# Kernel optimization log

Measured on AMD Instinct MI355X. Metric: run time of the kernel, lower is better.

Reference implementation:

```python
import jax, jax.numpy as jnp
import numpy as np

EPS = 1e-5

def _bn_train(x, gamma, beta):
    # BatchNorm2d in training mode: batch stats over (N,H,W), biased variance
    mean = jnp.mean(x, axis=(0, 2, 3), keepdims=True)
    var = jnp.mean((x - mean) ** 2, axis=(0, 2, 3), keepdims=True)
    xn = (x - mean) / jnp.sqrt(var + EPS)
    return xn * gamma[None, :, None, None] + beta[None, :, None, None]

def _bin_act(x):
    # forward: sign(x); backward: grad of clamp(x,-1,1) (STE)
    c = jnp.clip(x, -1.0, 1.0)
    return jax.lax.stop_gradient(jnp.sign(x) - c) + c

def _bin_conv(x, w_flat, out_chn, in_chn, k=3, stride=1, padding=1):
    w = w_flat.reshape(out_chn, in_chn, k, k)
    scale = jax.lax.stop_gradient(jnp.mean(jnp.abs(w), axis=(1, 2, 3), keepdims=True))
    cw = jnp.clip(w, -1.0, 1.0)
    bw = jax.lax.stop_gradient(scale * jnp.sign(w) - cw) + cw
    return jax.lax.conv_general_dilated(
        x, bw, window_strides=(stride, stride),
        padding=[(padding, padding), (padding, padding)],
        dimension_numbers=('NCHW', 'OIHW', 'NCHW'))

def _prelu(x, a):
    return jnp.where(x >= 0, x, a * x)

def setup_inputs() -> dict:
    key = jax.random.key(0)
    ks = jax.random.split(key, 4)
    C = 128
    x = jax.random.normal(ks[0], (64, C, 56, 56), dtype=jnp.float32)
    # HardBinaryConv stores weights as (n,1); init small, mixed-sign
    w1 = (jax.random.uniform(ks[1], (C * C * 9, 1), dtype=jnp.float32) - 0.5) * 0.002
    w2 = (jax.random.uniform(ks[2], (C * C * 9, 1), dtype=jnp.float32) - 0.5) * 0.002
    ones = jnp.ones((C,), jnp.float32)
    zeros = jnp.zeros((C,), jnp.float32)
    a = jnp.float32(0.25)
    return {
        'x': x,
        'bn1_g': ones, 'bn1_b': zeros,
        'w1': w1, 'prelu1_a': a,
        'bn2_g': ones, 'bn2_b': zeros,
        'w2': w2, 'prelu2_a': a,
        'bn3_g': ones, 'bn3_b': zeros,
        'prelu3_a': a,
    }

def reference(x, bn1_g, bn1_b, w1, prelu1_a, bn2_g, bn2_b, w2, prelu2_a, bn3_g, bn3_b, prelu3_a):
    C = x.shape[1]
    out = _bn_train(x, bn1_g, bn1_b)
    out = _bin_act(out)
    out = _prelu(_bin_conv(out, w1, C, C), prelu1_a)
    out = _bn_train(out, bn2_g, bn2_b)
    out = _bin_act(out)
    out = _bin_conv(out, w2, C, C)
    out = _prelu(out, prelu2_a)
    out = _bn_train(out, bn3_g, bn3_b)
    out = out + x  # identity shortcut (stride=1, in_planes==planes)
    out = _prelu(out, prelu3_a)
    return out
```

## Files before the change

kernel.cpp:

```cpp
#include <hip/hip_runtime.h>
#include <hip/hip_bf16.h>

typedef __attribute__((ext_vector_type(8))) short short8;
typedef __attribute__((ext_vector_type(4))) int i32x4;

#define HW     3136
#define M_TOT  200704
#define NSTEP  18
#define NBLK   1568

__device__ __forceinline__ void gload_lds16(const void* g, void* l) {
    __builtin_amdgcn_global_load_lds(
        (const __attribute__((address_space(1))) void*)g,
        (__attribute__((address_space(3))) void*)l, 16, 0, 0);
}

__global__ __launch_bounds__(256) void wsign_kernel(const float* __restrict__ w1,
                                                    const float* __restrict__ w2,
                                                    char* __restrict__ ws1,
                                                    char* __restrict__ ws2) {
    int i = blockIdx.x * 256 + threadIdx.x;
    const float* w = w1;
    char* wsz = ws1;
    if (i >= 147456) { i -= 147456; w = w2; wsz = ws2; }
    int e = i & 15, l = (i >> 4) & 63, f = (i >> 10) & 7, s = i >> 13;
    int cout = f * 16 + (l & 15);
    int k = s * 64 + (l >> 4) * 16 + e;
    int tap = k >> 7, cin = k & 127;
    float v = w[(cout * 128 + cin) * 9 + tap];
    wsz[i] = v > 0.f ? (char)1 : (v < 0.f ? (char)-1 : (char)0);
}

__global__ __launch_bounds__(256) void wscale_kernel(const float* __restrict__ w1,
                                                     const float* __restrict__ w2,
                                                     float* __restrict__ scale1,
                                                     float* __restrict__ scale2) {
    int o = blockIdx.x;
    const float* w = w1;
    float* scale = scale1;
    if (o >= 128) { o -= 128; w = w2; scale = scale2; }
    int t = threadIdx.x;
    float s = 0.f;
    for (int i = t; i < 1152; i += 256) s += fabsf(w[o * 1152 + i]);
    __shared__ float r1[256];
    r1[t] = s; __syncthreads();
    for (int off = 128; off > 0; off >>= 1) {
        if (t < off) r1[t] += r1[t + off];
        __syncthreads();
    }
    if (t == 0) scale[o] = r1[0] * (1.f / 1152.f);
}

__global__ __launch_bounds__(256) void stats_nchw_kernel(const float* __restrict__ x,
                                                         float* __restrict__ psum,
                                                         float* __restrict__ psq) {
    int bid = blockIdx.x;
    int n = bid >> 7, c = bid & 127;
    const float* p = x + (n * 128 + c) * HW;
    int t = threadIdx.x;
    float s = 0.f, q = 0.f;
    for (int i = t; i < HW; i += 256) { float v = p[i]; s += v; q += v * v; }
    __shared__ float r1[256], r2[256];
    r1[t] = s; r2[t] = q; __syncthreads();
    for (int off = 128; off > 0; off >>= 1) {
        if (t < off) { r1[t] += r1[t + off]; r2[t] += r2[t + off]; }
        __syncthreads();
    }
    if (t == 0) { psum[c * 64 + n] = r1[0]; psq[c * 64 + n] = r2[0]; }
}

__global__ void finalize_kernel(const float* __restrict__ psum, const float* __restrict__ psq,
                                int P, float* __restrict__ mean, float* __restrict__ rstd) {
    int c = threadIdx.x;
    if (c >= 128) return;
    float s = 0.f, q = 0.f;
    for (int j = 0; j < P; ++j) { s += psum[c * P + j]; q += psq[c * P + j]; }
    const float invN = 1.f / 200704.f;
    float m = s * invN;
    float var = q * invN - m * m;
    mean[c] = m;
    rstd[c] = 1.f / sqrtf(var + 1e-5f);
}

__global__ __launch_bounds__(256) void finalizeB_kernel(const float* __restrict__ psumB,
                                                        const float* __restrict__ psqB,
                                                        float* __restrict__ mean,
                                                        float* __restrict__ rstd) {
    int c = blockIdx.x, t = threadIdx.x;
    float s = 0.f, q = 0.f;
    for (int j = t; j < NBLK; j += 256) { s += psumB[c * NBLK + j]; q += psqB[c * NBLK + j]; }
    __shared__ float r1[256], r2[256];
    r1[t] = s; r2[t] = q; __syncthreads();
    for (int off = 128; off > 0; off >>= 1) {
        if (t < off) { r1[t] += r1[t + off]; r2[t] += r2[t + off]; }
        __syncthreads();
    }
    if (t == 0) {
        const float invN = 1.f / 200704.f;
        float m = r1[0] * invN;
        float var = r2[0] * invN - m * m;
        mean[c] = m;
        rstd[c] = 1.f / sqrtf(var + 1e-5f);
    }
}

__global__ __launch_bounds__(256) void act1_kernel(const float* __restrict__ x,
        const float* __restrict__ mean, const float* __restrict__ rstd,
        const float* __restrict__ g, const float* __restrict__ b,
        char* __restrict__ apad) {
    __shared__ float row[128 * 57];
    int blk = blockIdx.x;
    int n = blk / 58, hp = blk - n * 58;
    char* o = apad + (n * 58 + hp) * 58 * 128;
    int t = threadIdx.x;
    if (hp == 0 || hp == 57) {
        for (int i4 = t; i4 < 58 * 32; i4 += 256)
            *(char4*)(o + i4 * 4) = make_char4(0, 0, 0, 0);
        return;
    }
    const float* src = x + n * (128 * HW) + (hp - 1) * 56;
    for (int i = t; i < 128 * 56; i += 256) {
        int c = i / 56, w = i - c * 56;
        row[c * 57 + w] = src[c * HW + w];
    }
    __syncthreads();
    for (int i4 = t; i4 < 58 * 32; i4 += 256) {
        int wp = i4 >> 5;
        int c0 = (i4 & 31) * 4;
        char q[4] = {0, 0, 0, 0};
        if (wp >= 1 && wp <= 56) {
#pragma unroll
            for (int k = 0; k < 4; ++k) {
                int c = c0 + k;
                float xn = (row[c * 57 + wp - 1] - mean[c]) * rstd[c] * g[c] + b[c];
                q[k] = xn > 0.f ? 1 : (xn < 0.f ? -1 : 0);
            }
        }
        *(char4*)(o + wp * 128 + c0) = make_char4(q[0], q[1], q[2], q[3]);
    }
}

__global__ __launch_bounds__(256) void act2_kernel(const short* __restrict__ p1,
        const float* __restrict__ scale1, const float* __restrict__ a1ptr,
        const float* __restrict__ mean, const float* __restrict__ rstd,
        const float* __restrict__ g, const float* __restrict__ b,
        char* __restrict__ apad) {
    __shared__ float row[128 * 57];
    int blk = blockIdx.x;
    int n = blk / 58, hp = blk - n * 58;
    char* o = apad + (n * 58 + hp) * 58 * 128;
    int t = threadIdx.x;
    if (hp == 0 || hp == 57) {
        for (int i4 = t; i4 < 58 * 32; i4 += 256)
            *(char4*)(o + i4 * 4) = make_char4(0, 0, 0, 0);
        return;
    }
    float a1 = a1ptr[0];
    const short* src = p1 + n * HW + (hp - 1) * 56;
    for (int i = t; i < 128 * 56; i += 256) {
        int c = i / 56, w = i - c * 56;
        float v = scale1[c] * (float)src[(size_t)c * M_TOT + w];
        row[c * 57 + w] = v >= 0.f ? v : a1 * v;
    }
    __syncthreads();
    for (int i4 = t; i4 < 58 * 32; i4 += 256) {
        int wp = i4 >> 5;
        int c0 = (i4 & 31) * 4;
        char q[4] = {0, 0, 0, 0};
        if (wp >= 1 && wp <= 56) {
#pragma unroll
            for (int k = 0; k < 4; ++k) {
                int c = c0 + k;
                float xn = (row[c * 57 + wp - 1] - mean[c]) * rstd[c] * g[c] + b[c];
                q[k] = xn > 0.f ? 1 : (xn < 0.f ? -1 : 0);
            }
        }
        *(char4*)(o + wp * 128 + c0) = make_char4(q[0], q[1], q[2], q[3]);
    }
}

__global__ __launch_bounds__(256, 3) void conv_kernel(
        const char* __restrict__ apad,
        const char* __restrict__ wswz,
        const float* __restrict__ scale,
        const float* __restrict__ aptr,
        short* __restrict__ obuf,
        float* __restrict__ psumB,
        float* __restrict__ psqB) {
    __shared__ __align__(1024) char lds[16384];
    char* ldsA = lds;
    char* ldsB = lds + 8192;

    const int tid = threadIdx.x;
    const int lane = tid & 63;
    const int wid = tid >> 6;
    const int l15 = lane & 15;
    const int lq = lane >> 4;
    const int wr = wid >> 1;
    const int wc = wid & 1;

    int bid = blockIdx.x;
    int mblk = (bid & 7) * 196 + (bid >> 3);
    const int m0 = mblk * 128;

    const char* bsrc[2];
#pragma unroll
    for (int j = 0; j < 2; ++j) {
        int m = m0 + (j * 4 + wid) * 16 + l15;
        int n = m / HW;
        int r = m - n * HW;
        int h = r / 56;
        int w = r - h * 56;
        bsrc[j] = apad + (((n * 58 + h) * 58 + w) * 128 + lq * 16);
    }

    i32x4 acc[4][4];
#pragma unroll
    for (int i = 0; i < 4; ++i)
#pragma unroll
        for (int j = 0; j < 4; ++j)
            acc[i][j] = (i32x4){0, 0, 0, 0};

    for (int s = 0; s < NSTEP; ++s) {
        int tap = s >> 1;
        int dh = tap / 3;
        int dw = tap - dh * 3;
        int toff = (dh * 58 + dw) * 128 + (s & 1) * 64;
        const char* wsrc = wswz + s * 8192 + tid * 16;
        gload_lds16(wsrc,        ldsA + wid * 1024);
        gload_lds16(wsrc + 4096, ldsA + 4096 + wid * 1024);
        gload_lds16(bsrc[0] + toff, ldsB + wid * 1024);
        gload_lds16(bsrc[1] + toff, ldsB + 4096 + wid * 1024);
        __syncthreads();

        i32x4 af[4], bf[4];
#pragma unroll
        for (int ci = 0; ci < 4; ++ci)
            af[ci] = *(const i32x4*)(ldsA + (wr * 4 + ci) * 1024 + lane * 16);
#pragma unroll
        for (int mi = 0; mi < 4; ++mi)
            bf[mi] = *(const i32x4*)(ldsB + (wc * 4 + mi) * 1024 + lane * 16);
#pragma unroll
        for (int ci = 0; ci < 4; ++ci)
#pragma unroll
            for (int mi = 0; mi < 4; ++mi)
                acc[ci][mi] = __builtin_amdgcn_mfma_i32_16x16x64_i8(
                    af[ci], bf[mi], acc[ci][mi], 0, 0, 0);
        __syncthreads();
    }

    float alpha = aptr[0];
    float* partS = (float*)lds;
    float* partQ = (float*)(lds + 1024);
#pragma unroll
    for (int ci = 0; ci < 4; ++ci) {
        int cb = wr * 64 + ci * 16 + lq * 4;
        int mb = m0 + wc * 64 + l15;
#pragma unroll
        for (int r = 0; r < 4; ++r) {
            float sc = scale[cb + r];
            short* op = obuf + (size_t)(cb + r) * M_TOT + mb;
            float s = 0.f, q = 0.f;
#pragma unroll
            for (int mi = 0; mi < 4; ++mi) {
                int iv = acc[ci][mi][r];
                float v = (float)iv * sc;
                float pv = v >= 0.f ? v : alpha * v;
                op[mi * 16] = (short)iv;
                s += pv; q += pv * pv;
            }
#pragma unroll
            for (int msk = 1; msk <= 8; msk <<= 1) {
                s += __shfl_xor(s, msk, 64);
                q += __shfl_xor(q, msk, 64);
            }
            if (l15 == 0) { partS[wc * 128 + cb + r] = s; partQ[wc * 128 + cb + r] = q; }
        }
    }
    __syncthreads();
    if (tid < 128) {
        psumB[tid * NBLK + bid] = partS[tid] + partS[128 + tid];
        psqB [tid * NBLK + bid] = partQ[tid] + partQ[128 + tid];
    }
}

__global__ __launch_bounds__(256) void final_kernel(const short* __restrict__ p2,
        const float* __restrict__ scale2, const float* __restrict__ a2ptr,
        const float* __restrict__ x,
        const float* __restrict__ mean, const float* __restrict__ rstd,
        const float* __restrict__ g, const float* __restrict__ b,
        const float* __restrict__ a3ptr, float* __restrict__ out) {
    int bid = blockIdx.x;
    int n = bid >> 7, c = bid & 127;
    float sc = scale2[c], a2 = a2ptr[0];
    float m = mean[c], r = rstd[c], gg = g[c], bb = b[c], a3 = a3ptr[0];
    const short* pp = p2 + (size_t)c * M_TOT + n * HW;
    const float* xx = x + (n * 128 + c) * HW;
    float* oo = out + (n * 128 + c) * HW;
    int t = threadIdx.x;
    for (int i8 = t; i8 < 392; i8 += 256) {
        short8 v = *(const short8*)(pp + i8 * 8);
        float4 x0 = *(const float4*)(xx + i8 * 8);
        float4 x1 = *(const float4*)(xx + i8 * 8 + 4);
        float o[8];
#pragma unroll
        for (int k = 0; k < 8; ++k) {
            float pv = (float)v[k] * sc;
            pv = pv >= 0.f ? pv : a2 * pv;
            float xv = (k < 4) ? ((const float*)&x0)[k] : ((const float*)&x1)[k - 4];
            float val = (pv - m) * r * gg + bb + xv;
            o[k] = val >= 0.f ? val : a3 * val;
        }
        *(float4*)(oo + i8 * 8)     = make_float4(o[0], o[1], o[2], o[3]);
        *(float4*)(oo + i8 * 8 + 4) = make_float4(o[4], o[5], o[6], o[7]);
    }
}

extern "C" void kernel_launch(void* const* d_in, const int* in_sizes, int n_in,
                              void* d_out, int out_size, void* d_ws, size_t ws_size,
                              hipStream_t stream) {
    const float* x  = (const float*)d_in[0];
    const float* g1 = (const float*)d_in[1];
    const float* b1 = (const float*)d_in[2];
    const float* w1 = (const float*)d_in[3];
    const float* a1 = (const float*)d_in[4];
    const float* g2 = (const float*)d_in[5];
    const float* b2 = (const float*)d_in[6];
    const float* w2 = (const float*)d_in[7];
    const float* a2 = (const float*)d_in[8];
    const float* g3 = (const float*)d_in[9];
    const float* b3 = (const float*)d_in[10];
    const float* a3 = (const float*)d_in[11];
    float* out = (float*)d_out;
    char* ws = (char*)d_ws;

    float* scale1 = (float*)(ws);
    float* scale2 = (float*)(ws + 512);
    float* mean1  = (float*)(ws + 1024);
    float* rstd1  = (float*)(ws + 1536);
    float* mean2  = (float*)(ws + 2048);
    float* rstd2  = (float*)(ws + 2560);
    float* mean3  = (float*)(ws + 3072);
    float* rstd3  = (float*)(ws + 3584);
    float* psum   = (float*)(ws + 4096);
    float* psq    = (float*)(ws + 36864);
    float* psumB  = (float*)(ws + 69632);
    float* psqB   = (float*)(ws + 872448);
    char* wswz1   = (char*)(ws + 1675264);
    char* wswz2   = (char*)(ws + 1822720);
    char* apad8   = (char*)(ws + 1970176);
    short* buf2s  = (short*)(ws + 29528064);
    short* buf1s  = (short*)out;

    wscale_kernel<<<256, 256, 0, stream>>>(w1, w2, scale1, scale2);
    wsign_kernel<<<1152, 256, 0, stream>>>(w1, w2, wswz1, wswz2);

    stats_nchw_kernel<<<8192, 256, 0, stream>>>(x, psum, psq);
    finalize_kernel<<<1, 128, 0, stream>>>(psum, psq, 64, mean1, rstd1);
    act1_kernel<<<3712, 256, 0, stream>>>(x, mean1, rstd1, g1, b1, apad8);
    conv_kernel<<<1568, 256, 0, stream>>>(apad8, wswz1, scale1, a1, buf1s, psumB, psqB);

    finalizeB_kernel<<<128, 256, 0, stream>>>(psumB, psqB, mean2, rstd2);
    act2_kernel<<<3712, 256, 0, stream>>>(buf1s, scale1, a1, mean2, rstd2, g2, b2, apad8);
    conv_kernel<<<1568, 256, 0, stream>>>(apad8, wswz2, scale2, a2, buf2s, psumB, psqB);

    finalizeB_kernel<<<128, 256, 0, stream>>>(psumB, psqB, mean3, rstd3);
    final_kernel<<<8192, 256, 0, stream>>>(buf2s, scale2, a2, x, mean3, rstd3, g3, b3, a3, out);
}
```

Before: 297.6 us.

## Load conv MFMA operands directly from global into registers with double buffering

The int8 conv kernel no longer stages weight and activation tiles through LDS with async global-to-LDS loads and two barriers per step. Each wave now loads its MFMA fragments straight from global memory into registers, using two register sets so the next step's loads overlap the current step's MFMAs. This removes the per-step barriers and LDS traffic. In exchange, each wave issues redundant global loads (weights are re-read by both column waves, activations by both row waves) and register pressure rises, which may hurt occupancy at launch bounds of 3.

```diff
diff --git a/kernel.cpp b/kernel.cpp
--- a/kernel.cpp
+++ b/kernel.cpp
@@ -8,12 +8,6 @@
 #define M_TOT  200704
 #define NSTEP  18
 #define NBLK   1568
-
-__device__ __forceinline__ void gload_lds16(const void* g, void* l) {
-    __builtin_amdgcn_global_load_lds(
-        (const __attribute__((address_space(1))) void*)g,
-        (__attribute__((address_space(3))) void*)l, 16, 0, 0);
-}
 
 __global__ __launch_bounds__(256) void wsign_kernel(const float* __restrict__ w1,
                                                     const float* __restrict__ w2,
@@ -187,9 +181,8 @@
         short* __restrict__ obuf,
         float* __restrict__ psumB,
         float* __restrict__ psqB) {
-    __shared__ __align__(1024) char lds[16384];
-    char* ldsA = lds;
-    char* ldsB = lds + 8192;
+    __shared__ float partS[256];
+    __shared__ float partQ[256];
 
     const int tid = threadIdx.x;
     const int lane = tid & 63;
@@ -203,16 +196,17 @@
     int mblk = (bid & 7) * 196 + (bid >> 3);
     const int m0 = mblk * 128;
 
-    const char* bsrc[2];
-#pragma unroll
-    for (int j = 0; j < 2; ++j) {
-        int m = m0 + (j * 4 + wid) * 16 + l15;
+    const char* bptr[4];
+#pragma unroll
+    for (int mi = 0; mi < 4; ++mi) {
+        int m = m0 + wc * 64 + mi * 16 + l15;
         int n = m / HW;
         int r = m - n * HW;
         int h = r / 56;
         int w = r - h * 56;
-        bsrc[j] = apad + (((n * 58 + h) * 58 + w) * 128 + lq * 16);
-    }
+        bptr[mi] = apad + (((n * 58 + h) * 58 + w) * 128 + lq * 16);
+    }
+    const char* abase = wswz + wr * 4096 + lane * 16;
 
     i32x4 acc[4][4];
 #pragma unroll
@@ -221,37 +215,46 @@
         for (int j = 0; j < 4; ++j)
             acc[i][j] = (i32x4){0, 0, 0, 0};
 
-    for (int s = 0; s < NSTEP; ++s) {
-        int tap = s >> 1;
-        int dh = tap / 3;
-        int dw = tap - dh * 3;
-        int toff = (dh * 58 + dw) * 128 + (s & 1) * 64;
-        const char* wsrc = wswz + s * 8192 + tid * 16;
-        gload_lds16(wsrc,        ldsA + wid * 1024);
-        gload_lds16(wsrc + 4096, ldsA + 4096 + wid * 1024);
-        gload_lds16(bsrc[0] + toff, ldsB + wid * 1024);
-        gload_lds16(bsrc[1] + toff, ldsB + 4096 + wid * 1024);
-        __syncthreads();
-
-        i32x4 af[4], bf[4];
-#pragma unroll
-        for (int ci = 0; ci < 4; ++ci)
-            af[ci] = *(const i32x4*)(ldsA + (wr * 4 + ci) * 1024 + lane * 16);
-#pragma unroll
-        for (int mi = 0; mi < 4; ++mi)
-            bf[mi] = *(const i32x4*)(ldsB + (wc * 4 + mi) * 1024 + lane * 16);
-#pragma unroll
-        for (int ci = 0; ci < 4; ++ci)
-#pragma unroll
-            for (int mi = 0; mi < 4; ++mi)
-                acc[ci][mi] = __builtin_amdgcn_mfma_i32_16x16x64_i8(
-                    af[ci], bf[mi], acc[ci][mi], 0, 0, 0);
-        __syncthreads();
-    }
+    i32x4 afA[4], bfA[4], afB[4], bfB[4];
+
+#define LOADS(s, af, bf)                                                     \
+    {                                                                        \
+        int tap = (s) >> 1;                                                  \
+        int dh = tap / 3;                                                    \
+        int dw = tap - dh * 3;                                               \
+        int toff = (dh * 58 + dw) * 128 + ((s) & 1) * 64;                    \
+        const char* ab = abase + (s) * 8192;                                 \
+        af[0] = *(const i32x4*)(ab);                                         \
+        af[1] = *(const i32x4*)(ab + 1024);                                  \
+        af[2] = *(const i32x4*)(ab + 2048);                                  \
+        af[3] = *(const i32x4*)(ab + 3072);                                  \
+        bf[0] = *(const i32x4*)(bptr[0] + toff);                             \
+        bf[1] = *(const i32x4*)(bptr[1] + toff);                             \
+        bf[2] = *(const i32x4*)(bptr[2] + toff);                             \
+        bf[3] = *(const i32x4*)(bptr[3] + toff);                             \
+    }
+
+#define MFMAS(af, bf)                                                        \
+    {                                                                        \
+        _Pragma("unroll")                                                    \
+        for (int ci = 0; ci < 4; ++ci)                                       \
+            _Pragma("unroll")                                                \
+            for (int mi = 0; mi < 4; ++mi)                                   \
+                acc[ci][mi] = __builtin_amdgcn_mfma_i32_16x16x64_i8(         \
+                    af[ci], bf[mi], acc[ci][mi], 0, 0, 0);                   \
+    }
+
+    LOADS(0, afA, bfA);
+    for (int s = 0; s < NSTEP; s += 2) {
+        LOADS(s + 1, afB, bfB);
+        MFMAS(afA, bfA);
+        if (s + 2 < NSTEP) LOADS(s + 2, afA, bfA);
+        MFMAS(afB, bfB);
+    }
+#undef LOADS
+#undef MFMAS
 
     float alpha = aptr[0];
-    float* partS = (float*)lds;
-    float* partQ = (float*)(lds + 1024);
 #pragma unroll
     for (int ci = 0; ci < 4; ++ci) {
         int cb = wr * 64 + ci * 16 + lq * 4;
```

Result: slower. 362.7 us (+21.9%).
